# Kernel tuning notes

Measured on AMD Instinct MI355X. Metric: run time of the kernel, lower is better.

## Reference

```python
import jax, jax.numpy as jnp
import numpy as np

N = 100000      # nodes
K = 16          # neighbors per node
C_IN = 16
C1 = 64
C2 = 128
C_OUT = 40


def setup_inputs() -> dict:
    key = jax.random.key(0)
    ks = jax.random.split(key, 12)
    x = jax.random.normal(ks[0], (N, C_IN), dtype=jnp.float32)
    # kNN-style edge list: row = arange(N) repeated K times, col = neighbor ids
    row = jnp.repeat(jnp.arange(N, dtype=jnp.int32), K)
    col = jax.random.randint(ks[1], (N * K,), 0, N, dtype=jnp.int32)
    edge_index = jnp.stack([row, col], axis=0)  # [2, E]
    s = 0.02
    params = {
        'W1': jax.random.normal(ks[2], (2 * C_IN, C1), jnp.float32) * s,
        'b1': jnp.zeros((C1,), jnp.float32),
        'W2': jax.random.normal(ks[3], (C1, C1), jnp.float32) * s,
        'b2': jnp.zeros((C1,), jnp.float32),
        'W3': jax.random.normal(ks[4], (2 * C1, C2), jnp.float32) * s,
        'b3': jnp.zeros((C2,), jnp.float32),
        'W4': jax.random.normal(ks[5], (C2, C2), jnp.float32) * s,
        'b4': jnp.zeros((C2,), jnp.float32),
        'W5': jax.random.normal(ks[6], (C2, C2), jnp.float32) * s,
        'b5': jnp.zeros((C2,), jnp.float32),
        'W6': jax.random.normal(ks[7], (C2, C_OUT), jnp.float32) * s,
        'b6': jnp.zeros((C_OUT,), jnp.float32),
    }
    return {'x': x, 'edge_index': edge_index, **params}


def _edge_conv(x, row, col, Wa, ba, Wb, bb):
    # gather + diff + concat: [E, 2*C]
    xr = x[row]
    e = jnp.concatenate([xr, x[col] - xr], axis=-1)
    h = jax.nn.relu(e @ Wa + ba)
    return jax.nn.relu(h @ Wb + bb)


def reference(x, edge_index, W1, b1, W2, b2, W3, b3, W4, b4, W5, b5, W6, b6):
    row, col = edge_index[0], edge_index[1]
    h1 = _edge_conv(x, row, col, W1, b1, W2, b2)      # [E, 64]
    # as in the source, conv2 indexes the edge-feature tensor with node ids
    h2 = _edge_conv(h1, row, col, W3, b3, W4, b4)     # [E, 128]
    # max over the K neighbors of each node (edges grouped by row node)
    g = h2.reshape(N, K, C2).max(axis=1)              # [N, 128]
    out = jax.nn.relu(g @ W5 + b5) @ W6 + b6          # [N, out]
    return out
```

## Files before the change

kernel.cpp:

```cpp
#include <hip/hip_runtime.h>


#define NN 100000
#define KNB 16
#define EE (NN * KNB)

#define W2F 0
#define W3F 8
#define W4F 40
#define W5F 72
#define W6F 104
#define NFRAG 116

typedef float floatx4 __attribute__((ext_vector_type(4)));
typedef __bf16 bf16x8 __attribute__((ext_vector_type(8)));

static __device__ __forceinline__ unsigned f2bf_rne_u(float f) {
    unsigned u = __float_as_uint(f);
    return (u + 0x7FFFu + ((u >> 16) & 1u)) >> 16;
}
static __device__ __forceinline__ float bfu2f(unsigned h) {
    return __uint_as_float(h << 16);
}

static __device__ __forceinline__ void split_pack2(float a, float b,
                                                   unsigned& hp, unsigned& lp) {
    unsigned ua = __float_as_uint(a), ub = __float_as_uint(b);
    hp = __builtin_amdgcn_perm(ub, ua, 0x07060302u);
    float ra = a - __uint_as_float(ua & 0xFFFF0000u);
    float rb = b - __uint_as_float(ub & 0xFFFF0000u);
    unsigned la = __float_as_uint(ra), lb = __float_as_uint(rb);
    la = la + 0x7FFFu + ((la >> 16) & 1u);
    lb = lb + 0x7FFFu + ((lb >> 16) & 1u);
    lp = __builtin_amdgcn_perm(lb, la, 0x07060302u);
}

static __device__ __forceinline__ void split8(float4 f0, float4 f1,
                                              bf16x8& ah, bf16x8& al) {
    unsigned hd[4], ld[4];
    split_pack2(f0.x, f0.y, hd[0], ld[0]);
    split_pack2(f0.z, f0.w, hd[1], ld[1]);
    split_pack2(f1.x, f1.y, hd[2], ld[2]);
    split_pack2(f1.z, f1.w, hd[3], ld[3]);
    uint4 H = {hd[0], hd[1], hd[2], hd[3]};
    uint4 L = {ld[0], ld[1], ld[2], ld[3]};
    ah = __builtin_bit_cast(bf16x8, H);
    al = __builtin_bit_cast(bf16x8, L);
}

__global__ __launch_bounds__(256) void kw_kernel(
    const float* __restrict__ W2, const float* __restrict__ W3,
    const float* __restrict__ W4, const float* __restrict__ W5,
    const float* __restrict__ W6,
    unsigned short* __restrict__ WH, unsigned short* __restrict__ WL)
{
    int d = blockIdx.x * 256 + threadIdx.x;
    if (d >= NFRAG * 64) return;
    int f = d >> 6, l = d & 63, c = l & 15, q = l >> 4;
    float v[8];
    if (f < W3F) {
        int fx = f - W2F, kc = fx >> 2, nt = fx & 3;
        int k0 = kc * 32 + q * 8, n = nt * 16 + c;
#pragma unroll
        for (int j = 0; j < 8; ++j) v[j] = W2[(k0 + j) * 64 + n];
    } else if (f < W4F) {
        int fx = f - W3F, kc = fx >> 4, nt = fx & 15;
        int k0 = kc * 32 + q * 8, n = nt * 16 + c;
#pragma unroll
        for (int j = 0; j < 8; ++j) {
            int k = k0 + j;
            v[j] = (n < 128) ? (W3[k * 128 + n] - W3[(64 + k) * 128 + n])
                             : W3[(64 + k) * 128 + (n - 128)];
        }
    } else if (f < W5F) {
        int fx = f - W4F, kc = fx >> 3, nt = fx & 7;
        int k0 = kc * 32 + q * 8, n = nt * 16 + c;
#pragma unroll
        for (int j = 0; j < 8; ++j) v[j] = W4[(k0 + j) * 128 + n];
    } else if (f < W6F) {
        int fx = f - W5F, kc = fx >> 3, nt = fx & 7;
        int k0 = kc * 32 + q * 8, n = nt * 16 + c;
#pragma unroll
        for (int j = 0; j < 8; ++j) v[j] = W5[(k0 + j) * 128 + n];
    } else {
        int fx = f - W6F, kc = fx / 3, nt = fx % 3;
        int k0 = kc * 32 + q * 8, n = nt * 16 + c;
#pragma unroll
        for (int j = 0; j < 8; ++j)
            v[j] = (n < 40) ? W6[(k0 + j) * 40 + n] : 0.0f;
    }
    unsigned hs[8], ls[8];
#pragma unroll
    for (int j = 0; j < 8; ++j) {
        unsigned h = f2bf_rne_u(v[j]);
        float r = v[j] - bfu2f(h);
        hs[j] = h;
        ls[j] = f2bf_rne_u(r);
    }
    uint4 H, L;
    H.x = hs[0] | (hs[1] << 16); H.y = hs[2] | (hs[3] << 16);
    H.z = hs[4] | (hs[5] << 16); H.w = hs[6] | (hs[7] << 16);
    L.x = ls[0] | (ls[1] << 16); L.y = ls[2] | (ls[3] << 16);
    L.z = ls[4] | (ls[5] << 16); L.w = ls[6] | (ls[7] << 16);
    *(uint4*)(WH + (size_t)d * 8) = H;
    *(uint4*)(WL + (size_t)d * 8) = L;
}

__global__ __launch_bounds__(256) void k1_kernel(
    const float* __restrict__ x, const float* __restrict__ W1,
    const float* __restrict__ b1, float* __restrict__ A1, float* __restrict__ B1)
{
    int gid = blockIdx.x * 256 + threadIdx.x;
    int n = gid >> 6;
    int j = gid & 63;
    const float* xr = x + n * 16;
    float acc_a = b1[j];
    float acc_b = 0.0f;
#pragma unroll
    for (int k = 0; k < 16; ++k) {
        float xv = xr[k];
        float wt = W1[k * 64 + j];
        float wb = W1[(16 + k) * 64 + j];
        acc_a = fmaf(xv, wt - wb, acc_a);
        acc_b = fmaf(xv, wb, acc_b);
    }
    A1[n * 64 + j] = acc_a;
    B1[n * 64 + j] = acc_b;
}

__global__ __launch_bounds__(256) void k2_kernel(
    const int* __restrict__ col,
    const float* __restrict__ A1, const float* __restrict__ B1,
    const unsigned short* __restrict__ WH, const unsigned short* __restrict__ WL,
    const float* __restrict__ b2, const float* __restrict__ b3,
    float* __restrict__ A3, float* __restrict__ B3)
{
    __shared__ __align__(16) float tF[8 * 512];
    __shared__ __align__(16) float hF[8 * 512];
    const int t = threadIdx.x;
    const int i0 = blockIdx.x * 64;

    {
        const int row = t & 63, part = t >> 6;
        int i = i0 + row;
        int nn = i >> 4;
        int ci = col[i];
        const float* ar = A1 + (size_t)nn * 64 + part * 16;
        const float* br = B1 + (size_t)ci * 64 + part * 16;
        int mt = row >> 4, m = row & 15, kc = part >> 1;
        float* base = tF + (mt * 2 + kc) * 512 + m * 8;
#pragma unroll
        for (int h = 0; h < 2; ++h) {
            int qq = (part & 1) * 2 + h;
            float4 a0 = *(const float4*)(ar + h * 8);
            float4 b0 = *(const float4*)(br + h * 8);
            float4 a1 = *(const float4*)(ar + h * 8 + 4);
            float4 b1v = *(const float4*)(br + h * 8 + 4);
            float4 r0, r1;
            r0.x = fmaxf(a0.x + b0.x, 0.0f); r0.y = fmaxf(a0.y + b0.y, 0.0f);
            r0.z = fmaxf(a0.z + b0.z, 0.0f); r0.w = fmaxf(a0.w + b0.w, 0.0f);
            r1.x = fmaxf(a1.x + b1v.x, 0.0f); r1.y = fmaxf(a1.y + b1v.y, 0.0f);
            r1.z = fmaxf(a1.z + b1v.z, 0.0f); r1.w = fmaxf(a1.w + b1v.w, 0.0f);
            *(float4*)(base + qq * 128) = r0;
            *(float4*)(base + qq * 128 + 4) = r1;
        }
    }
    __syncthreads();

    const int w = __builtin_amdgcn_readfirstlane(t >> 6);
    const int lane = t & 63;

    floatx4 acc1[4];
#pragma unroll
    for (int nt = 0; nt < 4; ++nt) acc1[nt] = (floatx4){0.f, 0.f, 0.f, 0.f};
#pragma unroll
    for (int kc = 0; kc < 2; ++kc) {
        const float* ap = tF + (w * 2 + kc) * 512 + lane * 8;
        bf16x8 ah, al;
        split8(*(const float4*)ap, *(const float4*)(ap + 4), ah, al);
#pragma unroll
        for (int nt = 0; nt < 4; ++nt) {
            size_t fb = (size_t)(W2F + kc * 4 + nt) * 512 + lane * 8;
            bf16x8 bh = __builtin_bit_cast(bf16x8, *(const uint4*)(WH + fb));
            bf16x8 bl = __builtin_bit_cast(bf16x8, *(const uint4*)(WL + fb));
            acc1[nt] = __builtin_amdgcn_mfma_f32_16x16x32_bf16(ah, bh, acc1[nt], 0, 0, 0);
            acc1[nt] = __builtin_amdgcn_mfma_f32_16x16x32_bf16(ah, bl, acc1[nt], 0, 0, 0);
            acc1[nt] = __builtin_amdgcn_mfma_f32_16x16x32_bf16(al, bh, acc1[nt], 0, 0, 0);
        }
    }
    {
        const int qq = lane >> 4, cc = lane & 15;
#pragma unroll
        for (int nt = 0; nt < 4; ++nt) {
            float bv = b2[nt * 16 + cc];
            int colIdx = nt * 16 + cc;
            int kc2 = colIdx >> 5, q2 = (colIdx >> 3) & 3, jj = cc & 7;
            float* dst = hF + (w * 2 + kc2) * 512 + q2 * 128 + jj;
#pragma unroll
            for (int r = 0; r < 4; ++r)
                dst[(qq * 4 + r) * 8] = fmaxf(acc1[nt][r] + bv, 0.0f);
        }
    }
    floatx4 acc2[16];
#pragma unroll
    for (int nt = 0; nt < 16; ++nt) acc2[nt] = (floatx4){0.f, 0.f, 0.f, 0.f};
#pragma unroll
    for (int kc = 0; kc < 2; ++kc) {
        const float* ap = hF + (w * 2 + kc) * 512 + lane * 8;
        bf16x8 ah, al;
        split8(*(const float4*)ap, *(const float4*)(ap + 4), ah, al);
#pragma unroll
        for (int nt = 0; nt < 16; ++nt) {
            size_t fb = (size_t)(W3F + kc * 16 + nt) * 512 + lane * 8;
            bf16x8 bh = __builtin_bit_cast(bf16x8, *(const uint4*)(WH + fb));
            bf16x8 bl = __builtin_bit_cast(bf16x8, *(const uint4*)(WL + fb));
            acc2[nt] = __builtin_amdgcn_mfma_f32_16x16x32_bf16(ah, bh, acc2[nt], 0, 0, 0);
            acc2[nt] = __builtin_amdgcn_mfma_f32_16x16x32_bf16(ah, bl, acc2[nt], 0, 0, 0);
            acc2[nt] = __builtin_amdgcn_mfma_f32_16x16x32_bf16(al, bh, acc2[nt], 0, 0, 0);
        }
    }
    {
        const int qq = lane >> 4, cc = lane & 15;
#pragma unroll
        for (int nt = 0; nt < 16; ++nt) {
            int n = nt * 16 + cc;
            float bv = (n < 128) ? b3[n] : 0.0f;
#pragma unroll
            for (int r = 0; r < 4; ++r) {
                int i = i0 + w * 16 + qq * 4 + r;
                if (i < NN) {
                    float vv = acc2[nt][r];
                    if (n < 128) A3[(size_t)i * 128 + n] = vv + bv;
                    else         B3[(size_t)i * 128 + (n - 128)] = vv;
                }
            }
        }
    }
}

__global__ __launch_bounds__(256, 2) void k3_kernel(
    const int* __restrict__ col,
    const float* __restrict__ A3, const float* __restrict__ B3,
    const unsigned short* __restrict__ WH, const unsigned short* __restrict__ WL,
    const float* __restrict__ b4, float* __restrict__ g)
{
    __shared__ __align__(16) unsigned short wlds[32768];
    __shared__ __align__(16) float ashare[2048];
    const int t = threadIdx.x;
    const int lane = t & 63;
    const int w = t >> 6;
    const int m = lane & 15, q = lane >> 4;
    const int nodeB = blockIdx.x * 16;
    const int node0 = nodeB + w * 4;

    float4 braw[16];
#pragma unroll
    for (int ng = 0; ng < 2; ++ng) {
        const int c = col[(node0 + ng) * KNB + m];
        const float* br = B3 + (size_t)c * 128 + q * 8;
#pragma unroll
        for (int kc = 0; kc < 4; ++kc) {
            braw[ng * 8 + kc * 2]     = *(const float4*)(br + kc * 32);
            braw[ng * 8 + kc * 2 + 1] = *(const float4*)(br + kc * 32 + 4);
        }
    }
    {
        const float4* asrc = (const float4*)(A3 + (size_t)nodeB * 128);
        float4* adst = (float4*)ashare;
        adst[t]       = asrc[t];
        adst[t + 256] = asrc[t + 256];
        const uint4* hsrc = (const uint4*)WH;
        const uint4* lsrc = (const uint4*)WL;
        uint4* wdst = (uint4*)wlds;
#pragma unroll
        for (int i = 0; i < 8; ++i) wdst[t + i * 256]        = hsrc[t + i * 256];
#pragma unroll
        for (int i = 0; i < 8; ++i) wdst[2048 + t + i * 256] = lsrc[t + i * 256];
    }
    __syncthreads();

#pragma unroll
    for (int p = 0; p < 2; ++p) {
        bf16x8 aH[2][4], aL[2][4];
#pragma unroll
        for (int ng = 0; ng < 2; ++ng) {
            const float* ar = ashare + (w * 4 + p * 2 + ng) * 128 + q * 8;
#pragma unroll
            for (int kc = 0; kc < 4; ++kc) {
                float4 b0 = braw[ng * 8 + kc * 2];
                float4 b1 = braw[ng * 8 + kc * 2 + 1];
                float4 a0 = *(const float4*)(ar + kc * 32);
                float4 a1 = *(const float4*)(ar + kc * 32 + 4);
                float v0 = fmaxf(a0.x + b0.x, 0.0f), v1 = fmaxf(a0.y + b0.y, 0.0f);
                float v2 = fmaxf(a0.z + b0.z, 0.0f), v3 = fmaxf(a0.w + b0.w, 0.0f);
                float v4 = fmaxf(a1.x + b1.x, 0.0f), v5 = fmaxf(a1.y + b1.y, 0.0f);
                float v6 = fmaxf(a1.z + b1.z, 0.0f), v7 = fmaxf(a1.w + b1.w, 0.0f);
                uint4 H, L;
                split_pack2(v0, v1, H.x, L.x);
                split_pack2(v2, v3, H.y, L.y);
                split_pack2(v4, v5, H.z, L.z);
                split_pack2(v6, v7, H.w, L.w);
                aH[ng][kc] = __builtin_bit_cast(bf16x8, H);
                aL[ng][kc] = __builtin_bit_cast(bf16x8, L);
            }
        }
        if (p == 0) {
#pragma unroll
            for (int ng = 0; ng < 2; ++ng) {
                const int c = col[(node0 + 2 + ng) * KNB + m];
                const float* br = B3 + (size_t)c * 128 + q * 8;
#pragma unroll
                for (int kc = 0; kc < 4; ++kc) {
                    braw[ng * 8 + kc * 2]     = *(const float4*)(br + kc * 32);
                    braw[ng * 8 + kc * 2 + 1] = *(const float4*)(br + kc * 32 + 4);
                }
            }
        }
        floatx4 acc[2][8];
#pragma unroll
        for (int ng = 0; ng < 2; ++ng)
#pragma unroll
            for (int nt = 0; nt < 8; ++nt)
                acc[ng][nt] = (floatx4){0.0f, 0.0f, 0.0f, 0.0f};
#pragma unroll
        for (int kc = 0; kc < 4; ++kc) {
#pragma unroll
            for (int nt = 0; nt < 8; ++nt) {
                const int f = kc * 8 + nt;
                bf16x8 bh = __builtin_bit_cast(bf16x8,
                    *(const uint4*)(wlds + f * 512 + lane * 8));
                bf16x8 bl = __builtin_bit_cast(bf16x8,
                    *(const uint4*)(wlds + 16384 + f * 512 + lane * 8));
#pragma unroll
                for (int ng = 0; ng < 2; ++ng) {
                    acc[ng][nt] = __builtin_amdgcn_mfma_f32_16x16x32_bf16(
                        aH[ng][kc], bh, acc[ng][nt], 0, 0, 0);
                    acc[ng][nt] = __builtin_amdgcn_mfma_f32_16x16x32_bf16(
                        aH[ng][kc], bl, acc[ng][nt], 0, 0, 0);
                    acc[ng][nt] = __builtin_amdgcn_mfma_f32_16x16x32_bf16(
                        aL[ng][kc], bh, acc[ng][nt], 0, 0, 0);
                }
            }
        }
#pragma unroll
        for (int ng = 0; ng < 2; ++ng) {
            const int node = node0 + p * 2 + ng;
#pragma unroll
            for (int nt = 0; nt < 8; ++nt) {
                floatx4 a = acc[ng][nt];
                float mm = fmaxf(fmaxf(a[0], a[1]), fmaxf(a[2], a[3]));
                mm = fmaxf(mm, __shfl_xor(mm, 16));
                mm = fmaxf(mm, __shfl_xor(mm, 32));
                if (lane < 16) {
                    int ccol = nt * 16 + lane;
                    g[(size_t)node * 128 + ccol] = fmaxf(mm + b4[ccol], 0.0f);
                }
            }
        }
    }
}

__global__ __launch_bounds__(256) void k4_kernel(
    const float* __restrict__ g,
    const unsigned short* __restrict__ WH, const unsigned short* __restrict__ WL,
    const float* __restrict__ b5, const float* __restrict__ b6,
    float* __restrict__ out)
{
    __shared__ __align__(16) float gF[16 * 512];
    const int t = threadIdx.x;
    const int n0 = blockIdx.x * 64;

    {
        const int row = t & 63, part = t >> 6;
        int gn = n0 + row; if (gn >= NN) gn = NN - 1;
        const float* gr = g + (size_t)gn * 128 + part * 32;
        int mt = row >> 4, m = row & 15;
        float* base = gF + (mt * 4 + part) * 512 + m * 8;
#pragma unroll
        for (int qq = 0; qq < 4; ++qq) {
            *(float4*)(base + qq * 128)     = *(const float4*)(gr + qq * 8);
            *(float4*)(base + qq * 128 + 4) = *(const float4*)(gr + qq * 8 + 4);
        }
    }
    __syncthreads();

    const int w = __builtin_amdgcn_readfirstlane(t >> 6);
    const int lane = t & 63;

    floatx4 acc1[8];
#pragma unroll
    for (int nt = 0; nt < 8; ++nt) acc1[nt] = (floatx4){0.f, 0.f, 0.f, 0.f};
#pragma unroll
    for (int kc = 0; kc < 4; ++kc) {
        const float* ap = gF + (w * 4 + kc) * 512 + lane * 8;
        bf16x8 ah, al;
        split8(*(const float4*)ap, *(const float4*)(ap + 4), ah, al);
#pragma unroll
        for (int nt = 0; nt < 8; ++nt) {
            size_t fb = (size_t)(W5F + kc * 8 + nt) * 512 + lane * 8;
            bf16x8 bh = __builtin_bit_cast(bf16x8, *(const uint4*)(WH + fb));
            bf16x8 bl = __builtin_bit_cast(bf16x8, *(const uint4*)(WL + fb));
            acc1[nt] = __builtin_amdgcn_mfma_f32_16x16x32_bf16(ah, bh, acc1[nt], 0, 0, 0);
            acc1[nt] = __builtin_amdgcn_mfma_f32_16x16x32_bf16(ah, bl, acc1[nt], 0, 0, 0);
            acc1[nt] = __builtin_amdgcn_mfma_f32_16x16x32_bf16(al, bh, acc1[nt], 0, 0, 0);
        }
    }
    {
        const int qq = lane >> 4, cc = lane & 15;
#pragma unroll
        for (int nt = 0; nt < 8; ++nt) {
            float bv = b5[nt * 16 + cc];
            int colIdx = nt * 16 + cc;
            int kc2 = colIdx >> 5, q2 = (colIdx >> 3) & 3, jj = cc & 7;
            float* dst = gF + (w * 4 + kc2) * 512 + q2 * 128 + jj;
#pragma unroll
            for (int r = 0; r < 4; ++r)
                dst[(qq * 4 + r) * 8] = fmaxf(acc1[nt][r] + bv, 0.0f);
        }
    }
    floatx4 acc2[3];
#pragma unroll
    for (int nt = 0; nt < 3; ++nt) acc2[nt] = (floatx4){0.f, 0.f, 0.f, 0.f};
#pragma unroll
    for (int kc = 0; kc < 4; ++kc) {
        const float* ap = gF + (w * 4 + kc) * 512 + lane * 8;
        bf16x8 ah, al;
        split8(*(const float4*)ap, *(const float4*)(ap + 4), ah, al);
#pragma unroll
        for (int nt = 0; nt < 3; ++nt) {
            size_t fb = (size_t)(W6F + kc * 3 + nt) * 512 + lane * 8;
            bf16x8 bh = __builtin_bit_cast(bf16x8, *(const uint4*)(WH + fb));
            bf16x8 bl = __builtin_bit_cast(bf16x8, *(const uint4*)(WL + fb));
            acc2[nt] = __builtin_amdgcn_mfma_f32_16x16x32_bf16(ah, bh, acc2[nt], 0, 0, 0);
            acc2[nt] = __builtin_amdgcn_mfma_f32_16x16x32_bf16(ah, bl, acc2[nt], 0, 0, 0);
            acc2[nt] = __builtin_amdgcn_mfma_f32_16x16x32_bf16(al, bh, acc2[nt], 0, 0, 0);
        }
    }
    {
        const int qq = lane >> 4, cc = lane & 15;
#pragma unroll
        for (int nt = 0; nt < 3; ++nt) {
            int n = nt * 16 + cc;
            if (n < 40) {
                float bv = b6[n];
#pragma unroll
                for (int r = 0; r < 4; ++r) {
                    int i = n0 + w * 16 + qq * 4 + r;
                    if (i < NN)
                        out[(size_t)i * 40 + n] = acc2[nt][r] + bv;
                }
            }
        }
    }
}

extern "C" void kernel_launch(void* const* d_in, const int* in_sizes, int n_in,
                              void* d_out, int out_size, void* d_ws, size_t ws_size,
                              hipStream_t stream)
{
    const float* x  = (const float*)d_in[0];
    const int* ei   = (const int*)d_in[1];
    const int* col  = ei + EE;
    const float* W1 = (const float*)d_in[2];
    const float* b1 = (const float*)d_in[3];
    const float* W2 = (const float*)d_in[4];
    const float* b2 = (const float*)d_in[5];
    const float* W3 = (const float*)d_in[6];
    const float* b3 = (const float*)d_in[7];
    const float* W4 = (const float*)d_in[8];
    const float* b4 = (const float*)d_in[9];
    const float* W5 = (const float*)d_in[10];
    const float* b5 = (const float*)d_in[11];
    const float* W6 = (const float*)d_in[12];
    const float* b6 = (const float*)d_in[13];
    float* out = (float*)d_out;

    float* A1 = (float*)d_ws;
    float* B1 = A1 + (size_t)NN * 64;
    float* A3 = B1 + (size_t)NN * 64;
    float* B3 = A3 + (size_t)NN * 128;
    unsigned short* WH = (unsigned short*)(B3 + (size_t)NN * 128);
    unsigned short* WL = WH + NFRAG * 512;
    float* g  = A1;

    kw_kernel<<<(NFRAG * 64 + 255) / 256, 256, 0, stream>>>(W2, W3, W4, W5, W6, WH, WL);
    k1_kernel<<<NN * 64 / 256, 256, 0, stream>>>(x, W1, b1, A1, B1);
    k2_kernel<<<(NN + 63) / 64, 256, 0, stream>>>(col, A1, B1, WH, WL, b2, b3, A3, B3);
    k3_kernel<<<NN / 16, 256, 0, stream>>>(col, A3, B3,
                                           WH + (size_t)W4F * 512, WL + (size_t)W4F * 512,
                                           b4, g);
    k4_kernel<<<(NN + 63) / 64, 256, 0, stream>>>(g, WH, WL, b5, b6, out);
}
```

Before: 455.9 us.

## Fuse the final MLP head into the neighbor-max kernel

The k4 kernel is folded into k3. Each k3 block keeps its 16 pooled node vectors in registers, restages them in shared memory, and runs the W5 and W6 MFMA layers in place. Work is split across the four waves by output tile. This removes the global write and reread of the pooled tensor g and one kernel launch. In exchange it adds block barriers, idles one wave in the last layer, and reads W5 and W6 fragments from global memory in every block.

Measured after the change: 706.1 us. +54.9%, slower.

```diff
diff --git a/kernel.cpp b/kernel.cpp
--- a/kernel.cpp
+++ b/kernel.cpp
@@ -242,7 +242,8 @@
     const int* __restrict__ col,
     const float* __restrict__ A3, const float* __restrict__ B3,
     const unsigned short* __restrict__ WH, const unsigned short* __restrict__ WL,
-    const float* __restrict__ b4, float* __restrict__ g)
+    const float* __restrict__ b4, const float* __restrict__ b5,
+    const float* __restrict__ b6, float* __restrict__ out)
 {
     __shared__ __align__(16) unsigned short wlds[32768];
     __shared__ __align__(16) float ashare[2048];
@@ -269,8 +270,9 @@
         float4* adst = (float4*)ashare;
         adst[t]       = asrc[t];
         adst[t + 256] = asrc[t + 256];
-        const uint4* hsrc = (const uint4*)WH;
-        const uint4* lsrc = (const uint4*)WL;
+        const uint4* hsrc = (const uint4*)(WH + (size_t)W4F * 512 * 8 / 8);
+        const uint4* lsrc = (const uint4*)(WL + (size_t)W4F * 512);
+        hsrc = (const uint4*)(WH + (size_t)W4F * 512);
         uint4* wdst = (uint4*)wlds;
 #pragma unroll
         for (int i = 0; i < 8; ++i) wdst[t + i * 256]        = hsrc[t + i * 256];
@@ -278,6 +280,8 @@
         for (int i = 0; i < 8; ++i) wdst[2048 + t + i * 256] = lsrc[t + i * 256];
     }
     __syncthreads();
+
+    float gsave[4][8];
 
 #pragma unroll
     for (int p = 0; p < 2; ++p) {
@@ -344,112 +348,89 @@
         }
 #pragma unroll
         for (int ng = 0; ng < 2; ++ng) {
-            const int node = node0 + p * 2 + ng;
 #pragma unroll
             for (int nt = 0; nt < 8; ++nt) {
                 floatx4 a = acc[ng][nt];
                 float mm = fmaxf(fmaxf(a[0], a[1]), fmaxf(a[2], a[3]));
                 mm = fmaxf(mm, __shfl_xor(mm, 16));
                 mm = fmaxf(mm, __shfl_xor(mm, 32));
-                if (lane < 16) {
-                    int ccol = nt * 16 + lane;
-                    g[(size_t)node * 128 + ccol] = fmaxf(mm + b4[ccol], 0.0f);
-                }
-            }
-        }
-    }
-}
-
-__global__ __launch_bounds__(256) void k4_kernel(
-    const float* __restrict__ g,
-    const unsigned short* __restrict__ WH, const unsigned short* __restrict__ WL,
-    const float* __restrict__ b5, const float* __restrict__ b6,
-    float* __restrict__ out)
-{
-    __shared__ __align__(16) float gF[16 * 512];
-    const int t = threadIdx.x;
-    const int n0 = blockIdx.x * 64;
-
-    {
-        const int row = t & 63, part = t >> 6;
-        int gn = n0 + row; if (gn >= NN) gn = NN - 1;
-        const float* gr = g + (size_t)gn * 128 + part * 32;
-        int mt = row >> 4, m = row & 15;
-        float* base = gF + (mt * 4 + part) * 512 + m * 8;
-#pragma unroll
-        for (int qq = 0; qq < 4; ++qq) {
-            *(float4*)(base + qq * 128)     = *(const float4*)(gr + qq * 8);
-            *(float4*)(base + qq * 128 + 4) = *(const float4*)(gr + qq * 8 + 4);
-        }
-    }
-    __syncthreads();
-
-    const int w = __builtin_amdgcn_readfirstlane(t >> 6);
-    const int lane = t & 63;
-
-    floatx4 acc1[8];
-#pragma unroll
-    for (int nt = 0; nt < 8; ++nt) acc1[nt] = (floatx4){0.f, 0.f, 0.f, 0.f};
+                int ccol = nt * 16 + (lane & 15);
+                gsave[p * 2 + ng][nt] = fmaxf(mm + b4[ccol], 0.0f);
+            }
+        }
+    }
+
+    __syncthreads();
+    if (lane < 16) {
+        const int cc = lane;
+#pragma unroll
+        for (int pg = 0; pg < 4; ++pg) {
+            const int mloc = w * 4 + pg;
+#pragma unroll
+            for (int nt = 0; nt < 8; ++nt) {
+                int colI = nt * 16 + cc;
+                int kc2 = colI >> 5, q2 = (colI >> 3) & 3, jj = colI & 7;
+                ashare[kc2 * 512 + q2 * 128 + mloc * 8 + jj] = gsave[pg][nt];
+            }
+        }
+    }
+    __syncthreads();
+    floatx4 acc5[2];
+    acc5[0] = (floatx4){0.f, 0.f, 0.f, 0.f};
+    acc5[1] = (floatx4){0.f, 0.f, 0.f, 0.f};
 #pragma unroll
     for (int kc = 0; kc < 4; ++kc) {
-        const float* ap = gF + (w * 4 + kc) * 512 + lane * 8;
+        const float* ap = ashare + kc * 512 + lane * 8;
         bf16x8 ah, al;
         split8(*(const float4*)ap, *(const float4*)(ap + 4), ah, al);
 #pragma unroll
-        for (int nt = 0; nt < 8; ++nt) {
+        for (int ntl = 0; ntl < 2; ++ntl) {
+            int nt = w * 2 + ntl;
             size_t fb = (size_t)(W5F + kc * 8 + nt) * 512 + lane * 8;
             bf16x8 bh = __builtin_bit_cast(bf16x8, *(const uint4*)(WH + fb));
             bf16x8 bl = __builtin_bit_cast(bf16x8, *(const uint4*)(WL + fb));
-            acc1[nt] = __builtin_amdgcn_mfma_f32_16x16x32_bf16(ah, bh, acc1[nt], 0, 0, 0);
-            acc1[nt] = __builtin_amdgcn_mfma_f32_16x16x32_bf16(ah, bl, acc1[nt], 0, 0, 0);
-            acc1[nt] = __builtin_amdgcn_mfma_f32_16x16x32_bf16(al, bh, acc1[nt], 0, 0, 0);
-        }
-    }
+            acc5[ntl] = __builtin_amdgcn_mfma_f32_16x16x32_bf16(ah, bh, acc5[ntl], 0, 0, 0);
+            acc5[ntl] = __builtin_amdgcn_mfma_f32_16x16x32_bf16(ah, bl, acc5[ntl], 0, 0, 0);
+            acc5[ntl] = __builtin_amdgcn_mfma_f32_16x16x32_bf16(al, bh, acc5[ntl], 0, 0, 0);
+        }
+    }
+    __syncthreads();
     {
         const int qq = lane >> 4, cc = lane & 15;
 #pragma unroll
-        for (int nt = 0; nt < 8; ++nt) {
+        for (int ntl = 0; ntl < 2; ++ntl) {
+            int nt = w * 2 + ntl;
             float bv = b5[nt * 16 + cc];
-            int colIdx = nt * 16 + cc;
-            int kc2 = colIdx >> 5, q2 = (colIdx >> 3) & 3, jj = cc & 7;
-            float* dst = gF + (w * 4 + kc2) * 512 + q2 * 128 + jj;
+            int colI = nt * 16 + cc;
+            int kc2 = colI >> 5, q2 = (colI >> 3) & 3, jj = cc & 7;
+            float* dst = ashare + kc2 * 512 + q2 * 128 + jj;
 #pragma unroll
             for (int r = 0; r < 4; ++r)
-                dst[(qq * 4 + r) * 8] = fmaxf(acc1[nt][r] + bv, 0.0f);
-        }
-    }
-    floatx4 acc2[3];
-#pragma unroll
-    for (int nt = 0; nt < 3; ++nt) acc2[nt] = (floatx4){0.f, 0.f, 0.f, 0.f};
-#pragma unroll
-    for (int kc = 0; kc < 4; ++kc) {
-        const float* ap = gF + (w * 4 + kc) * 512 + lane * 8;
-        bf16x8 ah, al;
-        split8(*(const float4*)ap, *(const float4*)(ap + 4), ah, al);
-#pragma unroll
-        for (int nt = 0; nt < 3; ++nt) {
-            size_t fb = (size_t)(W6F + kc * 3 + nt) * 512 + lane * 8;
+                dst[(qq * 4 + r) * 8] = fmaxf(acc5[ntl][r] + bv, 0.0f);
+        }
+    }
+    __syncthreads();
+    if (w < 3) {
+        floatx4 acc6 = (floatx4){0.f, 0.f, 0.f, 0.f};
+#pragma unroll
+        for (int kc = 0; kc < 4; ++kc) {
+            const float* ap = ashare + kc * 512 + lane * 8;
+            bf16x8 ah, al;
+            split8(*(const float4*)ap, *(const float4*)(ap + 4), ah, al);
+            size_t fb = (size_t)(W6F + kc * 3 + w) * 512 + lane * 8;
             bf16x8 bh = __builtin_bit_cast(bf16x8, *(const uint4*)(WH + fb));
             bf16x8 bl = __builtin_bit_cast(bf16x8, *(const uint4*)(WL + fb));
-            acc2[nt] = __builtin_amdgcn_mfma_f32_16x16x32_bf16(ah, bh, acc2[nt], 0, 0, 0);
-            acc2[nt] = __builtin_amdgcn_mfma_f32_16x16x32_bf16(ah, bl, acc2[nt], 0, 0, 0);
-            acc2[nt] = __builtin_amdgcn_mfma_f32_16x16x32_bf16(al, bh, acc2[nt], 0, 0, 0);
-        }
-    }
-    {
+            acc6 = __builtin_amdgcn_mfma_f32_16x16x32_bf16(ah, bh, acc6, 0, 0, 0);
+            acc6 = __builtin_amdgcn_mfma_f32_16x16x32_bf16(ah, bl, acc6, 0, 0, 0);
+            acc6 = __builtin_amdgcn_mfma_f32_16x16x32_bf16(al, bh, acc6, 0, 0, 0);
+        }
         const int qq = lane >> 4, cc = lane & 15;
-#pragma unroll
-        for (int nt = 0; nt < 3; ++nt) {
-            int n = nt * 16 + cc;
-            if (n < 40) {
-                float bv = b6[n];
-#pragma unroll
-                for (int r = 0; r < 4; ++r) {
-                    int i = n0 + w * 16 + qq * 4 + r;
-                    if (i < NN)
-                        out[(size_t)i * 40 + n] = acc2[nt][r] + bv;
-                }
-            }
+        int n = w * 16 + cc;
+        if (n < 40) {
+            float bv = b6[n];
+#pragma unroll
+            for (int r = 0; r < 4; ++r)
+                out[(size_t)(nodeB + qq * 4 + r) * 40 + n] = acc6[r] + bv;
         }
     }
 }
@@ -481,13 +462,9 @@
     float* B3 = A3 + (size_t)NN * 128;
     unsigned short* WH = (unsigned short*)(B3 + (size_t)NN * 128);
     unsigned short* WL = WH + NFRAG * 512;
-    float* g  = A1;
 
     kw_kernel<<<(NFRAG * 64 + 255) / 256, 256, 0, stream>>>(W2, W3, W4, W5, W6, WH, WL);
     k1_kernel<<<NN * 64 / 256, 256, 0, stream>>>(x, W1, b1, A1, B1);
     k2_kernel<<<(NN + 63) / 64, 256, 0, stream>>>(col, A1, B1, WH, WL, b2, b3, A3, B3);
-    k3_kernel<<<NN / 16, 256, 0, stream>>>(col, A3, B3,
-                                           WH + (size_t)W4F * 512, WL + (size_t)W4F * 512,
-                                           b4, g);
-    k4_kernel<<<(NN + 63) / 64, 256, 0, stream>>>(g, WH, WL, b5, b6, out);
-}
+    k3_kernel<<<NN / 16, 256, 0, stream>>>(col, A3, B3, WH, WL, b4, b5, b6, out);
+}
```
